# Kernel tuning notes

Hardware: AMD Instinct MI355X
Metric: run time of the kernel (lower is better)

The kernel has to match this reference:

```python
import jax, jax.numpy as jnp
import numpy as np

BATCH = 16384
D_MODEL = 2048
N_EXPERT = 64


def setup_inputs() -> dict:
    key = jax.random.key(0)
    kx, kw = jax.random.split(key)
    x = jax.random.normal(kx, (BATCH, D_MODEL), dtype=jnp.float32)
    # nn.Linear(d_model, n_expert, bias=False) -> weight [n_expert, d_model]
    w_gate = jax.random.normal(kw, (N_EXPERT, D_MODEL), dtype=jnp.float32) * (1.0 / np.sqrt(D_MODEL))
    return {"x": x, "w_gate": w_gate}


def reference(x, w_gate):
    # logits = x @ W^T : [batch, n_expert]
    logits = jnp.einsum("bd,ed->be", x, w_gate)
    idx = jnp.argmax(logits, axis=-1)                       # [batch]
    mask = jax.nn.one_hot(idx, logits.shape[-1], dtype=jnp.float32)  # [batch, nE]
    scores = jnp.sum(mask * logits, axis=-1, keepdims=True)  # [batch, 1]
    return (idx, scores, mask)
```

## Files before the change

### kernel.cpp

```cpp
#include <hip/hip_runtime.h>


typedef float  f32x4  __attribute__((ext_vector_type(4)));
typedef short  bf16x8 __attribute__((ext_vector_type(8)));

constexpr int BATCH = 16384;
constexpr int DM    = 2048;
constexpr int NE    = 64;
constexpr int BM    = 32;
constexpr int NT    = 256;


__device__ __forceinline__ void split_bf16(float f, unsigned short& hi, unsigned short& lo) {
    unsigned u  = __float_as_uint(f);
    unsigned h  = (u + 0x8000u) >> 16;
    float    hf = __uint_as_float(h << 16);
    unsigned l  = __float_as_uint(f - hf) >> 16;
    hi = (unsigned short)h;
    lo = (unsigned short)l;
}

__global__ __launch_bounds__(256, 1)
void wconv_kernel(const float* __restrict__ w, unsigned short* __restrict__ wf) {
    int i  = blockIdx.x * 256 + threadIdx.x;
    int ks = i >> 11;
    int n  = (i >> 9) & 3;
    int l  = (i >> 3) & 63;
    int j  = i & 7;
    int e  = n * 16 + (l & 15);
    int k  = ks * 32 + (l >> 4) * 8 + j;
    float v = w[(size_t)e * DM + k];
    unsigned short hi, lo;
    split_bf16(v, hi, lo);
    int base = ((ks * 2 + 0) * 4 + n) * 512 + l * 8 + j;
    wf[base]        = hi;
    wf[base + 2048] = lo;
}

struct BSet { bf16x8 v[8]; };

__global__ __launch_bounds__(NT, 2)
void gate_kernel(const float* __restrict__ x,
                 const unsigned short* __restrict__ wf,
                 float* __restrict__ out) {
    __shared__ alignas(16) float xs[4][16 * 32 * 4];
    __shared__ float lg[BM][NE + 1];
    __shared__ int   s_idx[BM];

    const int t     = threadIdx.x;
    const int lane  = t & 63;
    const int q     = t >> 6;
    const int row0  = blockIdx.x * BM;
    const int phase = (blockIdx.x & 15) << 1;

    f32x4 acc[2][4];
    #pragma unroll
    for (int h = 0; h < 2; ++h)
        #pragma unroll
        for (int n = 0; n < 4; ++n) acc[h][n] = (f32x4){0.f, 0.f, 0.f, 0.f};

    auto kbOf = [&](int c) { return ((c + phase) >> 1) & 15; };

    auto stage_x = [&](int c, int b) {
        const int h = c & 1;
        const float* xg = x + (size_t)(row0 + h * 16) * DM + kbOf(c) * 128;
        #pragma unroll
        for (int i = 0; i < 2; ++i) {
            int d    = i * NT + t;
            int r    = d >> 5;
            int sdst = d & 31;
            int ssrc = sdst ^ ((r & 7) << 2);
            __builtin_amdgcn_global_load_lds(
                (const __attribute__((address_space(1))) void*)(xg + (size_t)r * DM + ssrc * 4),
                (__attribute__((address_space(3))) void*)(&xs[b][d * 4]),
                16, 0, 0);
        }
    };

    auto load_b = [&](int c, BSet& B) {
        int ks = kbOf(c) * 4 + q;
        const unsigned short* wg = wf + (size_t)ks * 4096 + lane * 8;
        #pragma unroll
        for (int f = 0; f < 8; ++f)
            B.v[f] = *(const bf16x8*)(wg + (size_t)f * 512);
    };

    auto compute = [&](int b, int hh, const BSet& B) {
        const int rA = lane & 15;
        const int s0 = q * 8 + ((lane >> 4) << 1);
        const int xr = (rA & 7) << 2;
        f32x4 a0 = *(const f32x4*)&xs[b][(rA * 32 + ((s0 + 0) ^ xr)) * 4];
        f32x4 a1 = *(const f32x4*)&xs[b][(rA * 32 + ((s0 + 1) ^ xr)) * 4];
        bf16x8 ahi, alo;
        #pragma unroll
        for (int j = 0; j < 8; ++j) {
            float f = (j < 4) ? a0[j] : a1[j - 4];
            unsigned short h, l;
            split_bf16(f, h, l);
            ahi[j] = (short)h;
            alo[j] = (short)l;
        }
        #pragma unroll
        for (int n = 0; n < 4; ++n) {
            acc[hh][n] = __builtin_amdgcn_mfma_f32_16x16x32_bf16(ahi, B.v[0 + n], acc[hh][n], 0, 0, 0);
            acc[hh][n] = __builtin_amdgcn_mfma_f32_16x16x32_bf16(ahi, B.v[4 + n], acc[hh][n], 0, 0, 0);
            acc[hh][n] = __builtin_amdgcn_mfma_f32_16x16x32_bf16(alo, B.v[0 + n], acc[hh][n], 0, 0, 0);
        }
    };

    BSet BA, BB;

    load_b(0, BA);
    stage_x(0, 0);
    stage_x(1, 1);
    stage_x(2, 2);
    asm volatile("s_waitcnt vmcnt(4)" ::: "memory");
    __builtin_amdgcn_sched_barrier(0);
    __builtin_amdgcn_s_barrier();

    #pragma unroll 1
    for (int c = 0; c < 28; c += 4) {
        load_b(c + 2, BB);
        stage_x(c + 3, (c + 3) & 3);
        asm volatile("s_waitcnt vmcnt(12)" ::: "memory");
        __builtin_amdgcn_sched_barrier(0);
        compute((c + 0) & 3, 0, BA);
        __builtin_amdgcn_s_barrier();

        stage_x(c + 4, (c + 4) & 3);
        asm volatile("s_waitcnt vmcnt(12)" ::: "memory");
        __builtin_amdgcn_sched_barrier(0);
        compute((c + 1) & 3, 1, BA);
        __builtin_amdgcn_s_barrier();

        load_b(c + 4, BA);
        stage_x(c + 5, (c + 5) & 3);
        asm volatile("s_waitcnt vmcnt(12)" ::: "memory");
        __builtin_amdgcn_sched_barrier(0);
        compute((c + 2) & 3, 0, BB);
        __builtin_amdgcn_s_barrier();

        stage_x(c + 6, (c + 6) & 3);
        asm volatile("s_waitcnt vmcnt(12)" ::: "memory");
        __builtin_amdgcn_sched_barrier(0);
        compute((c + 3) & 3, 1, BB);
        __builtin_amdgcn_s_barrier();
    }

    load_b(30, BB);
    stage_x(31, 3);
    asm volatile("s_waitcnt vmcnt(12)" ::: "memory");
    __builtin_amdgcn_sched_barrier(0);
    compute(0, 0, BA);
    __builtin_amdgcn_s_barrier();

    compute(1, 1, BA);
    __builtin_amdgcn_s_barrier();

    asm volatile("s_waitcnt vmcnt(2)" ::: "memory");
    __builtin_amdgcn_sched_barrier(0);
    compute(2, 0, BB);
    __builtin_amdgcn_s_barrier();

    asm volatile("s_waitcnt vmcnt(0)" ::: "memory");
    __builtin_amdgcn_sched_barrier(0);
    compute(3, 1, BB);
    __syncthreads();

    const int rb = (lane >> 4) << 2;
    const int cb = lane & 15;
    if (q == 0) {
        #pragma unroll
        for (int h = 0; h < 2; ++h)
            #pragma unroll
            for (int n = 0; n < 4; ++n)
                #pragma unroll
                for (int j = 0; j < 4; ++j)
                    lg[h * 16 + rb + j][n * 16 + cb] = acc[h][n][j];
    }
    __syncthreads();
    if (q == 1) {
        #pragma unroll
        for (int h = 0; h < 2; ++h)
            #pragma unroll
            for (int n = 0; n < 4; ++n)
                #pragma unroll
                for (int j = 0; j < 4; ++j)
                    lg[h * 16 + rb + j][n * 16 + cb] += acc[h][n][j];
    }
    __syncthreads();
    if (q == 2) {
        #pragma unroll
        for (int h = 0; h < 2; ++h)
            #pragma unroll
            for (int n = 0; n < 4; ++n)
                #pragma unroll
                for (int j = 0; j < 4; ++j)
                    lg[h * 16 + rb + j][n * 16 + cb] += acc[h][n][j];
    }
    __syncthreads();
    if (q == 3) {
        #pragma unroll
        for (int h = 0; h < 2; ++h)
            #pragma unroll
            for (int n = 0; n < 4; ++n)
                #pragma unroll
                for (int j = 0; j < 4; ++j)
                    lg[h * 16 + rb + j][n * 16 + cb] += acc[h][n][j];
    }
    __syncthreads();

    if (t < BM) {
        float m  = lg[t][0];
        int   mi = 0;
        #pragma unroll
        for (int e = 1; e < NE; ++e) {
            float v = lg[t][e];
            if (v > m) { m = v; mi = e; }
        }
        s_idx[t] = mi;
        out[row0 + t]         = (float)mi;
        out[BATCH + row0 + t] = m;
    }
    __syncthreads();

    float* mask = out + 2 * (size_t)BATCH;
    int r  = t >> 3;
    int c0 = (t & 7) * 8;
    int mi = s_idx[r];
    #pragma unroll
    for (int i = 0; i < 2; ++i) {
        f32x4 v;
        #pragma unroll
        for (int j = 0; j < 4; ++j) v[j] = (c0 + i * 4 + j == mi) ? 1.0f : 0.0f;
        *(f32x4*)&mask[(size_t)(row0 + r) * NE + c0 + i * 4] = v;
    }
}

extern "C" void kernel_launch(void* const* d_in, const int* in_sizes, int n_in,
                              void* d_out, int out_size, void* d_ws, size_t ws_size,
                              hipStream_t stream) {
    const float* x = (const float*)d_in[0];
    const float* w = (const float*)d_in[1];
    float* out     = (float*)d_out;
    unsigned short* wf = (unsigned short*)d_ws;

    wconv_kernel<<<dim3(512), dim3(256), 0, stream>>>(w, wf);
    gate_kernel<<<dim3(BATCH / BM), dim3(NT), 0, stream>>>(x, wf, out);
}
```

Measured before the change: 37.11 us.

## Fuse weight bf16 split into gate kernel, drop separate conversion launch

Removes the separate wconv kernel that pre-split the fp32 gate weights into hi/lo bf16 fragments in workspace. The gate kernel now loads raw fp32 weights directly and performs the hi/lo split in registers before each pair of MFMA compute steps. This removes one kernel launch and a workspace round trip. In exchange, every block redoes the weight conversion, reads twice the weight bytes through a strided fp32 access pattern, and may use more registers under its two-blocks-per-CU launch bound.

```diff
diff --git a/kernel.cpp b/kernel.cpp
--- a/kernel.cpp
+++ b/kernel.cpp
@@ -9,7 +9,6 @@
 constexpr int NE    = 64;
 constexpr int BM    = 32;
 constexpr int NT    = 256;
-
 
 __device__ __forceinline__ void split_bf16(float f, unsigned short& hi, unsigned short& lo) {
     unsigned u  = __float_as_uint(f);
@@ -20,28 +19,11 @@
     lo = (unsigned short)l;
 }
 
-__global__ __launch_bounds__(256, 1)
-void wconv_kernel(const float* __restrict__ w, unsigned short* __restrict__ wf) {
-    int i  = blockIdx.x * 256 + threadIdx.x;
-    int ks = i >> 11;
-    int n  = (i >> 9) & 3;
-    int l  = (i >> 3) & 63;
-    int j  = i & 7;
-    int e  = n * 16 + (l & 15);
-    int k  = ks * 32 + (l >> 4) * 8 + j;
-    float v = w[(size_t)e * DM + k];
-    unsigned short hi, lo;
-    split_bf16(v, hi, lo);
-    int base = ((ks * 2 + 0) * 4 + n) * 512 + l * 8 + j;
-    wf[base]        = hi;
-    wf[base + 2048] = lo;
-}
-
 struct BSet { bf16x8 v[8]; };
 
 __global__ __launch_bounds__(NT, 2)
 void gate_kernel(const float* __restrict__ x,
-                 const unsigned short* __restrict__ wf,
+                 const float* __restrict__ w,
                  float* __restrict__ out) {
     __shared__ alignas(16) float xs[4][16 * 32 * 4];
     __shared__ float lg[BM][NE + 1];
@@ -77,12 +59,31 @@
         }
     };
 
-    auto load_b = [&](int c, BSet& B) {
+    auto load_raw = [&](int c, f32x4* R) {
         int ks = kbOf(c) * 4 + q;
-        const unsigned short* wg = wf + (size_t)ks * 4096 + lane * 8;
-        #pragma unroll
-        for (int f = 0; f < 8; ++f)
-            B.v[f] = *(const bf16x8*)(wg + (size_t)f * 512);
+        const float* wp = w + (size_t)(lane & 15) * DM + ks * 32 + ((lane >> 4) << 3);
+        #pragma unroll
+        for (int n = 0; n < 4; ++n) {
+            R[n * 2 + 0] = *(const f32x4*)(wp + (size_t)n * 16 * DM);
+            R[n * 2 + 1] = *(const f32x4*)(wp + (size_t)n * 16 * DM + 4);
+        }
+    };
+
+    auto mksplit = [&](const f32x4* R, BSet& S) {
+        #pragma unroll
+        for (int n = 0; n < 4; ++n) {
+            bf16x8 hi, lo;
+            #pragma unroll
+            for (int j = 0; j < 8; ++j) {
+                float f = (j < 4) ? R[n * 2][j] : R[n * 2 + 1][j - 4];
+                unsigned short h, l;
+                split_bf16(f, h, l);
+                hi[j] = (short)h;
+                lo[j] = (short)l;
+            }
+            S.v[n]     = hi;
+            S.v[4 + n] = lo;
+        }
     };
 
     auto compute = [&](int b, int hh, const BSet& B) {
@@ -108,9 +109,10 @@
         }
     };
 
-    BSet BA, BB;
-
-    load_b(0, BA);
+    f32x4 rawA[8], rawB[8];
+    BSet  S;
+
+    load_raw(0, rawA);
     stage_x(0, 0);
     stage_x(1, 1);
     stage_x(2, 2);
@@ -120,51 +122,55 @@
 
     #pragma unroll 1
     for (int c = 0; c < 28; c += 4) {
-        load_b(c + 2, BB);
+        load_raw(c + 2, rawB);
         stage_x(c + 3, (c + 3) & 3);
         asm volatile("s_waitcnt vmcnt(12)" ::: "memory");
         __builtin_amdgcn_sched_barrier(0);
-        compute((c + 0) & 3, 0, BA);
+        mksplit(rawA, S);
+        compute((c + 0) & 3, 0, S);
         __builtin_amdgcn_s_barrier();
 
         stage_x(c + 4, (c + 4) & 3);
         asm volatile("s_waitcnt vmcnt(12)" ::: "memory");
         __builtin_amdgcn_sched_barrier(0);
-        compute((c + 1) & 3, 1, BA);
-        __builtin_amdgcn_s_barrier();
-
-        load_b(c + 4, BA);
+        compute((c + 1) & 3, 1, S);
+        __builtin_amdgcn_s_barrier();
+
+        load_raw(c + 4, rawA);
         stage_x(c + 5, (c + 5) & 3);
         asm volatile("s_waitcnt vmcnt(12)" ::: "memory");
         __builtin_amdgcn_sched_barrier(0);
-        compute((c + 2) & 3, 0, BB);
+        mksplit(rawB, S);
+        compute((c + 2) & 3, 0, S);
         __builtin_amdgcn_s_barrier();
 
         stage_x(c + 6, (c + 6) & 3);
         asm volatile("s_waitcnt vmcnt(12)" ::: "memory");
         __builtin_amdgcn_sched_barrier(0);
-        compute((c + 3) & 3, 1, BB);
-        __builtin_amdgcn_s_barrier();
-    }
-
-    load_b(30, BB);
+        compute((c + 3) & 3, 1, S);
+        __builtin_amdgcn_s_barrier();
+    }
+
+    load_raw(30, rawB);
     stage_x(31, 3);
     asm volatile("s_waitcnt vmcnt(12)" ::: "memory");
     __builtin_amdgcn_sched_barrier(0);
-    compute(0, 0, BA);
-    __builtin_amdgcn_s_barrier();
-
-    compute(1, 1, BA);
+    mksplit(rawA, S);
+    compute(0, 0, S);
+    __builtin_amdgcn_s_barrier();
+
+    compute(1, 1, S);
     __builtin_amdgcn_s_barrier();
 
     asm volatile("s_waitcnt vmcnt(2)" ::: "memory");
     __builtin_amdgcn_sched_barrier(0);
-    compute(2, 0, BB);
+    mksplit(rawB, S);
+    compute(2, 0, S);
     __builtin_amdgcn_s_barrier();
 
     asm volatile("s_waitcnt vmcnt(0)" ::: "memory");
     __builtin_amdgcn_sched_barrier(0);
-    compute(3, 1, BB);
+    compute(3, 1, S);
     __syncthreads();
 
     const int rb = (lane >> 4) << 2;
@@ -243,8 +249,6 @@
     const float* x = (const float*)d_in[0];
     const float* w = (const float*)d_in[1];
     float* out     = (float*)d_out;
-    unsigned short* wf = (unsigned short*)d_ws;
-
-    wconv_kernel<<<dim3(512), dim3(256), 0, stream>>>(w, wf);
-    gate_kernel<<<dim3(BATCH / BM), dim3(NT), 0, stream>>>(x, wf, out);
+
+    gate_kernel<<<dim3(BATCH / BM), dim3(NT), 0, stream>>>(x, w, out);
 }
```

New measurement: 47.65 us. +28.4%, slower.

## Shrink row tile to 16 rows with 16-chunk pipeline and higher occupancy

Applied to the files above, without the earlier changes.

Halves the per-block row tile from 32 to 16, doubling the grid to 1024 blocks. Each block now loops over 16 K-chunks with one accumulator set, and the pipeline is restructured with B-operand loads every chunk. Launch bounds are raised to allow four blocks per CU to improve latency hiding. Because each block now reuses the gate weights for only 16 rows, total weight reads from L2 double, and the initial barrier before the main loop is removed.

```diff
diff --git a/kernel.cpp b/kernel.cpp
--- a/kernel.cpp
+++ b/kernel.cpp
@@ -7,8 +7,9 @@
 constexpr int BATCH = 16384;
 constexpr int DM    = 2048;
 constexpr int NE    = 64;
-constexpr int BM    = 32;
+constexpr int BM    = 16;
 constexpr int NT    = 256;
+constexpr int NCH   = 16;
 
 
 __device__ __forceinline__ void split_bf16(float f, unsigned short& hi, unsigned short& lo) {
@@ -39,7 +40,7 @@
 
 struct BSet { bf16x8 v[8]; };
 
-__global__ __launch_bounds__(NT, 2)
+__global__ __launch_bounds__(NT, 4)
 void gate_kernel(const float* __restrict__ x,
                  const unsigned short* __restrict__ wf,
                  float* __restrict__ out) {
@@ -51,19 +52,16 @@
     const int lane  = t & 63;
     const int q     = t >> 6;
     const int row0  = blockIdx.x * BM;
-    const int phase = (blockIdx.x & 15) << 1;
-
-    f32x4 acc[2][4];
+    const int phase = blockIdx.x & 15;
+
+    f32x4 acc[4];
     #pragma unroll
-    for (int h = 0; h < 2; ++h)
-        #pragma unroll
-        for (int n = 0; n < 4; ++n) acc[h][n] = (f32x4){0.f, 0.f, 0.f, 0.f};
-
-    auto kbOf = [&](int c) { return ((c + phase) >> 1) & 15; };
+    for (int n = 0; n < 4; ++n) acc[n] = (f32x4){0.f, 0.f, 0.f, 0.f};
+
+    auto kbOf = [&](int c) { return (c + phase) & 15; };
 
     auto stage_x = [&](int c, int b) {
-        const int h = c & 1;
-        const float* xg = x + (size_t)(row0 + h * 16) * DM + kbOf(c) * 128;
+        const float* xg = x + (size_t)row0 * DM + kbOf(c) * 128;
         #pragma unroll
         for (int i = 0; i < 2; ++i) {
             int d    = i * NT + t;
@@ -85,7 +83,7 @@
             B.v[f] = *(const bf16x8*)(wg + (size_t)f * 512);
     };
 
-    auto compute = [&](int b, int hh, const BSet& B) {
+    auto compute = [&](int b, const BSet& B) {
         const int rA = lane & 15;
         const int s0 = q * 8 + ((lane >> 4) << 1);
         const int xr = (rA & 7) << 2;
@@ -102,9 +100,9 @@
         }
         #pragma unroll
         for (int n = 0; n < 4; ++n) {
-            acc[hh][n] = __builtin_amdgcn_mfma_f32_16x16x32_bf16(ahi, B.v[0 + n], acc[hh][n], 0, 0, 0);
-            acc[hh][n] = __builtin_amdgcn_mfma_f32_16x16x32_bf16(ahi, B.v[4 + n], acc[hh][n], 0, 0, 0);
-            acc[hh][n] = __builtin_amdgcn_mfma_f32_16x16x32_bf16(alo, B.v[0 + n], acc[hh][n], 0, 0, 0);
+            acc[n] = __builtin_amdgcn_mfma_f32_16x16x32_bf16(ahi, B.v[0 + n], acc[n], 0, 0, 0);
+            acc[n] = __builtin_amdgcn_mfma_f32_16x16x32_bf16(ahi, B.v[4 + n], acc[n], 0, 0, 0);
+            acc[n] = __builtin_amdgcn_mfma_f32_16x16x32_bf16(alo, B.v[0 + n], acc[n], 0, 0, 0);
         }
     };
 
@@ -114,99 +112,76 @@
     stage_x(0, 0);
     stage_x(1, 1);
     stage_x(2, 2);
-    asm volatile("s_waitcnt vmcnt(4)" ::: "memory");
-    __builtin_amdgcn_sched_barrier(0);
-    __builtin_amdgcn_s_barrier();
 
     #pragma unroll 1
-    for (int c = 0; c < 28; c += 4) {
-        load_b(c + 2, BB);
+    for (int c = 0; c < 12; c += 2) {
+        load_b(c + 1, BB);
         stage_x(c + 3, (c + 3) & 3);
         asm volatile("s_waitcnt vmcnt(12)" ::: "memory");
         __builtin_amdgcn_sched_barrier(0);
-        compute((c + 0) & 3, 0, BA);
+        compute(c & 3, BA);
         __builtin_amdgcn_s_barrier();
 
+        load_b(c + 2, BA);
         stage_x(c + 4, (c + 4) & 3);
         asm volatile("s_waitcnt vmcnt(12)" ::: "memory");
         __builtin_amdgcn_sched_barrier(0);
-        compute((c + 1) & 3, 1, BA);
+        compute((c + 1) & 3, BB);
         __builtin_amdgcn_s_barrier();
-
-        load_b(c + 4, BA);
-        stage_x(c + 5, (c + 5) & 3);
-        asm volatile("s_waitcnt vmcnt(12)" ::: "memory");
-        __builtin_amdgcn_sched_barrier(0);
-        compute((c + 2) & 3, 0, BB);
-        __builtin_amdgcn_s_barrier();
-
-        stage_x(c + 6, (c + 6) & 3);
-        asm volatile("s_waitcnt vmcnt(12)" ::: "memory");
-        __builtin_amdgcn_sched_barrier(0);
-        compute((c + 3) & 3, 1, BB);
-        __builtin_amdgcn_s_barrier();
-    }
-
-    load_b(30, BB);
-    stage_x(31, 3);
+    }
+    load_b(13, BB);
+    stage_x(15, 3);
     asm volatile("s_waitcnt vmcnt(12)" ::: "memory");
     __builtin_amdgcn_sched_barrier(0);
-    compute(0, 0, BA);
+    compute(0, BA);
     __builtin_amdgcn_s_barrier();
-
-    compute(1, 1, BA);
+    load_b(14, BA);
+    asm volatile("s_waitcnt vmcnt(10)" ::: "memory");
+    __builtin_amdgcn_sched_barrier(0);
+    compute(1, BB);
     __builtin_amdgcn_s_barrier();
-
-    asm volatile("s_waitcnt vmcnt(2)" ::: "memory");
-    __builtin_amdgcn_sched_barrier(0);
-    compute(2, 0, BB);
+    load_b(15, BB);
+    asm volatile("s_waitcnt vmcnt(8)" ::: "memory");
+    __builtin_amdgcn_sched_barrier(0);
+    compute(2, BA);
     __builtin_amdgcn_s_barrier();
-
     asm volatile("s_waitcnt vmcnt(0)" ::: "memory");
     __builtin_amdgcn_sched_barrier(0);
-    compute(3, 1, BB);
+    compute(3, BB);
     __syncthreads();
 
     const int rb = (lane >> 4) << 2;
     const int cb = lane & 15;
     if (q == 0) {
         #pragma unroll
-        for (int h = 0; h < 2; ++h)
-            #pragma unroll
-            for (int n = 0; n < 4; ++n)
-                #pragma unroll
-                for (int j = 0; j < 4; ++j)
-                    lg[h * 16 + rb + j][n * 16 + cb] = acc[h][n][j];
+        for (int n = 0; n < 4; ++n)
+            #pragma unroll
+            for (int j = 0; j < 4; ++j)
+                lg[rb + j][n * 16 + cb] = acc[n][j];
     }
     __syncthreads();
     if (q == 1) {
         #pragma unroll
-        for (int h = 0; h < 2; ++h)
-            #pragma unroll
-            for (int n = 0; n < 4; ++n)
-                #pragma unroll
-                for (int j = 0; j < 4; ++j)
-                    lg[h * 16 + rb + j][n * 16 + cb] += acc[h][n][j];
+        for (int n = 0; n < 4; ++n)
+            #pragma unroll
+            for (int j = 0; j < 4; ++j)
+                lg[rb + j][n * 16 + cb] += acc[n][j];
     }
     __syncthreads();
     if (q == 2) {
         #pragma unroll
-        for (int h = 0; h < 2; ++h)
-            #pragma unroll
-            for (int n = 0; n < 4; ++n)
-                #pragma unroll
-                for (int j = 0; j < 4; ++j)
-                    lg[h * 16 + rb + j][n * 16 + cb] += acc[h][n][j];
+        for (int n = 0; n < 4; ++n)
+            #pragma unroll
+            for (int j = 0; j < 4; ++j)
+                lg[rb + j][n * 16 + cb] += acc[n][j];
     }
     __syncthreads();
     if (q == 3) {
         #pragma unroll
-        for (int h = 0; h < 2; ++h)
-            #pragma unroll
-            for (int n = 0; n < 4; ++n)
-                #pragma unroll
-                for (int j = 0; j < 4; ++j)
-                    lg[h * 16 + rb + j][n * 16 + cb] += acc[h][n][j];
+        for (int n = 0; n < 4; ++n)
+            #pragma unroll
+            for (int j = 0; j < 4; ++j)
+                lg[rb + j][n * 16 + cb] += acc[n][j];
     }
     __syncthreads();
 
@@ -225,16 +200,13 @@
     __syncthreads();
 
     float* mask = out + 2 * (size_t)BATCH;
-    int r  = t >> 3;
-    int c0 = (t & 7) * 8;
+    int r  = t >> 4;
+    int c0 = (t & 15) * 4;
     int mi = s_idx[r];
+    f32x4 v;
     #pragma unroll
-    for (int i = 0; i < 2; ++i) {
-        f32x4 v;
-        #pragma unroll
-        for (int j = 0; j < 4; ++j) v[j] = (c0 + i * 4 + j == mi) ? 1.0f : 0.0f;
-        *(f32x4*)&mask[(size_t)(row0 + r) * NE + c0 + i * 4] = v;
-    }
+    for (int j = 0; j < 4; ++j) v[j] = (c0 + j == mi) ? 1.0f : 0.0f;
+    *(f32x4*)&mask[(size_t)(row0 + r) * NE + c0] = v;
 }
 
 extern "C" void kernel_launch(void* const* d_in, const int* in_sizes, int n_in,
```

After: 53.70 us. 44.7% more time.

## Deepen software pipeline to 8 LDS x-stages and triple-buffered weight registers

Applied to the files above, without the earlier changes.

Doubles the LDS staging ring for x tiles from 4 to 8 buffers and rotates three register sets of weight fragments instead of two, so more global loads stay in flight ahead of the MFMA compute. The loop is restructured around k-blocks with explicit vmcnt waits plus a barrier before each compute step. This is meant to hide memory latency in a bandwidth-bound GEMV-like gate. In exchange it uses more LDS and more VGPRs, which may lower occupancy below the two blocks per CU targeted by the launch bounds.

```diff
diff --git a/kernel.cpp b/kernel.cpp
--- a/kernel.cpp
+++ b/kernel.cpp
@@ -39,19 +39,24 @@
 
 struct BSet { bf16x8 v[8]; };
 
+#define WAITN(N) do { asm volatile("s_waitcnt vmcnt(" #N ")" ::: "memory"); \
+                      __builtin_amdgcn_sched_barrier(0); \
+                      __builtin_amdgcn_s_barrier(); \
+                      __builtin_amdgcn_sched_barrier(0); } while (0)
+
 __global__ __launch_bounds__(NT, 2)
 void gate_kernel(const float* __restrict__ x,
                  const unsigned short* __restrict__ wf,
                  float* __restrict__ out) {
-    __shared__ alignas(16) float xs[4][16 * 32 * 4];
+    __shared__ alignas(16) float xs[8][16 * 32 * 4];
     __shared__ float lg[BM][NE + 1];
     __shared__ int   s_idx[BM];
 
-    const int t     = threadIdx.x;
-    const int lane  = t & 63;
-    const int q     = t >> 6;
-    const int row0  = blockIdx.x * BM;
-    const int phase = (blockIdx.x & 15) << 1;
+    const int t    = threadIdx.x;
+    const int lane = t & 63;
+    const int q    = t >> 6;
+    const int row0 = blockIdx.x * BM;
+    const int pph  = blockIdx.x & 15;
 
     f32x4 acc[2][4];
     #pragma unroll
@@ -59,11 +64,12 @@
         #pragma unroll
         for (int n = 0; n < 4; ++n) acc[h][n] = (f32x4){0.f, 0.f, 0.f, 0.f};
 
-    auto kbOf = [&](int c) { return ((c + phase) >> 1) & 15; };
-
-    auto stage_x = [&](int c, int b) {
+    auto pb = [&](int p) { return (p + pph) & 15; };
+
+    auto stage_x = [&](int c) {
         const int h = c & 1;
-        const float* xg = x + (size_t)(row0 + h * 16) * DM + kbOf(c) * 128;
+        const float* xg = x + (size_t)(row0 + h * 16) * DM + pb(c >> 1) * 128;
+        float* dst = &xs[c & 7][0];
         #pragma unroll
         for (int i = 0; i < 2; ++i) {
             int d    = i * NT + t;
@@ -72,25 +78,26 @@
             int ssrc = sdst ^ ((r & 7) << 2);
             __builtin_amdgcn_global_load_lds(
                 (const __attribute__((address_space(1))) void*)(xg + (size_t)r * DM + ssrc * 4),
-                (__attribute__((address_space(3))) void*)(&xs[b][d * 4]),
+                (__attribute__((address_space(3))) void*)(dst + d * 4),
                 16, 0, 0);
         }
     };
 
-    auto load_b = [&](int c, BSet& B) {
-        int ks = kbOf(c) * 4 + q;
+    auto load_b = [&](int p, BSet& B) {
+        int ks = pb(p) * 4 + q;
         const unsigned short* wg = wf + (size_t)ks * 4096 + lane * 8;
         #pragma unroll
         for (int f = 0; f < 8; ++f)
             B.v[f] = *(const bf16x8*)(wg + (size_t)f * 512);
     };
 
-    auto compute = [&](int b, int hh, const BSet& B) {
+    auto compute = [&](int c, int hh, const BSet& B) {
+        const float* src = &xs[c & 7][0];
         const int rA = lane & 15;
         const int s0 = q * 8 + ((lane >> 4) << 1);
         const int xr = (rA & 7) << 2;
-        f32x4 a0 = *(const f32x4*)&xs[b][(rA * 32 + ((s0 + 0) ^ xr)) * 4];
-        f32x4 a1 = *(const f32x4*)&xs[b][(rA * 32 + ((s0 + 1) ^ xr)) * 4];
+        f32x4 a0 = *(const f32x4*)(src + (rA * 32 + ((s0 + 0) ^ xr)) * 4);
+        f32x4 a1 = *(const f32x4*)(src + (rA * 32 + ((s0 + 1) ^ xr)) * 4);
         bf16x8 ahi, alo;
         #pragma unroll
         for (int j = 0; j < 8; ++j) {
@@ -108,63 +115,62 @@
         }
     };
 
-    BSet BA, BB;
-
-    load_b(0, BA);
-    stage_x(0, 0);
-    stage_x(1, 1);
-    stage_x(2, 2);
-    asm volatile("s_waitcnt vmcnt(4)" ::: "memory");
-    __builtin_amdgcn_sched_barrier(0);
-    __builtin_amdgcn_s_barrier();
+    BSet S0, S1, S2;
+
+    load_b(0, S0);
+    stage_x(0);
+    stage_x(1);
+    load_b(1, S1);
+    stage_x(2);
+    stage_x(3);
 
     #pragma unroll 1
-    for (int c = 0; c < 28; c += 4) {
-        load_b(c + 2, BB);
-        stage_x(c + 3, (c + 3) & 3);
-        asm volatile("s_waitcnt vmcnt(12)" ::: "memory");
-        __builtin_amdgcn_sched_barrier(0);
-        compute((c + 0) & 3, 0, BA);
-        __builtin_amdgcn_s_barrier();
-
-        stage_x(c + 4, (c + 4) & 3);
-        asm volatile("s_waitcnt vmcnt(12)" ::: "memory");
-        __builtin_amdgcn_sched_barrier(0);
-        compute((c + 1) & 3, 1, BA);
-        __builtin_amdgcn_s_barrier();
-
-        load_b(c + 4, BA);
-        stage_x(c + 5, (c + 5) & 3);
-        asm volatile("s_waitcnt vmcnt(12)" ::: "memory");
-        __builtin_amdgcn_sched_barrier(0);
-        compute((c + 2) & 3, 0, BB);
-        __builtin_amdgcn_s_barrier();
-
-        stage_x(c + 6, (c + 6) & 3);
-        asm volatile("s_waitcnt vmcnt(12)" ::: "memory");
-        __builtin_amdgcn_sched_barrier(0);
-        compute((c + 3) & 3, 1, BB);
-        __builtin_amdgcn_s_barrier();
-    }
-
-    load_b(30, BB);
-    stage_x(31, 3);
-    asm volatile("s_waitcnt vmcnt(12)" ::: "memory");
-    __builtin_amdgcn_sched_barrier(0);
-    compute(0, 0, BA);
-    __builtin_amdgcn_s_barrier();
-
-    compute(1, 1, BA);
-    __builtin_amdgcn_s_barrier();
-
-    asm volatile("s_waitcnt vmcnt(2)" ::: "memory");
-    __builtin_amdgcn_sched_barrier(0);
-    compute(2, 0, BB);
-    __builtin_amdgcn_s_barrier();
-
-    asm volatile("s_waitcnt vmcnt(0)" ::: "memory");
-    __builtin_amdgcn_sched_barrier(0);
-    compute(3, 1, BB);
+    for (int p = 0; p < 12; p += 3) {
+        const int c = 2 * p;
+        load_b(p + 2, S2);
+        stage_x(c + 4);
+        WAITN(24);
+        compute(c + 0, 0, S0);
+        stage_x(c + 5);
+        WAITN(24);
+        compute(c + 1, 1, S0);
+        load_b(p + 3, S0);
+        stage_x(c + 6);
+        WAITN(24);
+        compute(c + 2, 0, S1);
+        stage_x(c + 7);
+        WAITN(24);
+        compute(c + 3, 1, S1);
+        load_b(p + 4, S1);
+        stage_x(c + 8);
+        WAITN(24);
+        compute(c + 4, 0, S2);
+        stage_x(c + 9);
+        WAITN(24);
+        compute(c + 5, 1, S2);
+    }
+    load_b(14, S2);
+    stage_x(28);
+    WAITN(24);
+    compute(24, 0, S0);
+    stage_x(29);
+    WAITN(24);
+    compute(25, 1, S0);
+    load_b(15, S0);
+    stage_x(30);
+    WAITN(24);
+    compute(26, 0, S1);
+    stage_x(31);
+    WAITN(24);
+    compute(27, 1, S1);
+    WAITN(14);
+    compute(28, 0, S2);
+    WAITN(12);
+    compute(29, 1, S2);
+    WAITN(2);
+    compute(30, 0, S0);
+    WAITN(0);
+    compute(31, 1, S0);
     __syncthreads();
 
     const int rb = (lane >> 4) << 2;
```

Measured after the change: 38.63 us. +4.1%, slower.
